# Optimization experiments

Hardware: AMD Instinct MI355X
Metric: run time of the kernel (lower is better)

Reference implementation:

```python
import jax, jax.numpy as jnp
import numpy as np

EPS = 1e-6
H, HKV, D = 32, 8, 64          # heads, kv heads, head_dim
E, TOP_K, FF = 8, 2, 1024      # experts, top-k, expert intermediate
HID = 2048


def rms_norm(x, w):
    xf = x.astype(jnp.float32)
    var = jnp.mean(xf * xf, axis=-1, keepdims=True)
    return (w * (xf * jax.lax.rsqrt(var + EPS)).astype(x.dtype))


def rotate_half(x):
    x1, x2 = jnp.split(x, 2, axis=-1)
    return jnp.concatenate([-x2, x1], axis=-1)


def apply_rope(q, k, cos, sin):
    # cos/sin: [B,S,rd] -> [B,1,S,rd]
    cos = cos[:, None, :, :]
    sin = sin[:, None, :, :]
    rd = cos.shape[-1]
    q_rot, q_pass = q[..., :rd], q[..., rd:]
    k_rot, k_pass = k[..., :rd], k[..., rd:]
    q_emb = q_rot * cos + rotate_half(q_rot) * sin
    k_emb = k_rot * cos + rotate_half(k_rot) * sin
    return (jnp.concatenate([q_emb, q_pass], -1), jnp.concatenate([k_emb, k_pass], -1))


def attention(x, cos, sin, wq, wk, wv, wo):
    B, S, _ = x.shape
    q = (x @ wq).reshape(B, S, H, D).transpose(0, 2, 1, 3)      # [B,H,S,D]
    k = (x @ wk).reshape(B, S, HKV, D).transpose(0, 2, 1, 3)    # [B,Hk,S,D]
    v = (x @ wv).reshape(B, S, HKV, D).transpose(0, 2, 1, 3)
    q, k = apply_rope(q, k, cos, sin)
    rep = H // HKV
    k = jnp.repeat(k, rep, axis=1)
    v = jnp.repeat(v, rep, axis=1)
    scale = D ** -0.5
    scores = jnp.einsum('bhqd,bhkd->bhqk', q, k) * scale
    causal = jnp.triu(jnp.full((S, S), -jnp.inf, dtype=scores.dtype), k=1)
    scores = scores + causal
    probs = jax.nn.softmax(scores.astype(jnp.float32), axis=-1).astype(q.dtype)
    out = jnp.einsum('bhqk,bhkd->bhqd', probs, v)
    out = out.transpose(0, 2, 1, 3).reshape(B, S, H * D)
    return out @ wo


def moe(x, gate_w, corr_bias, w1, w2, w3):
    B, S, Dm = x.shape
    xf = x.reshape(-1, Dm)                                      # [T, Dm]
    T = xf.shape[0]
    logits = xf @ gate_w                                        # [T, E]
    rw = jax.nn.sigmoid(logits.astype(jnp.float32))
    scores = rw + corr_bias
    _, sel = jax.lax.top_k(scores, TOP_K)                       # [T, k]
    tw = jnp.take_along_axis(rw, sel, axis=-1)
    tw = tw / jnp.sum(tw, axis=-1, keepdims=True)
    # dense [T, E] combine weights (zero for unselected experts)
    cw = jnp.zeros((T, E), dtype=xf.dtype).at[jnp.arange(T)[:, None], sel].set(tw.astype(xf.dtype))
    # run every expert densely, combine with sparse weights (same math as gather/scatter loop)
    h = jax.nn.silu(jnp.einsum('td,edf->etf', xf, w1)) * jnp.einsum('td,edf->etf', xf, w3)
    eo = jnp.einsum('etf,efd->etd', h, w2)                      # [E, T, Dm]
    out = jnp.einsum('etd,te->td', eo, cw)
    return out.reshape(B, S, Dm)


def setup_inputs() -> dict:
    key = jax.random.key(0)
    ks = jax.random.split(key, 16)
    s = 0.02
    return {
        'hidden_states': jax.random.normal(ks[0], (2, 1024, HID), jnp.float32),
        'cos': jax.random.uniform(ks[1], (2, 1024, D), jnp.float32),
        'sin': jax.random.uniform(ks[2], (2, 1024, D), jnp.float32),
        'ln1_w': jnp.ones((HID,), jnp.float32),
        'ln2_w': jnp.ones((HID,), jnp.float32),
        'wq': jax.random.normal(ks[3], (HID, H * D), jnp.float32) * s,
        'wk': jax.random.normal(ks[4], (HID, HKV * D), jnp.float32) * s,
        'wv': jax.random.normal(ks[5], (HID, HKV * D), jnp.float32) * s,
        'wo': jax.random.normal(ks[6], (H * D, HID), jnp.float32) * s,
        'gate_w': jax.random.normal(ks[7], (HID, E), jnp.float32) * s,
        'corr_bias': jnp.zeros((E,), jnp.float32),
        'w1': jax.random.normal(ks[8], (E, HID, FF), jnp.float32) * s,
        'w2': jax.random.normal(ks[9], (E, FF, HID), jnp.float32) * s,
        'w3': jax.random.normal(ks[10], (E, HID, FF), jnp.float32) * s,
    }


def reference(hidden_states, cos, sin, ln1_w, ln2_w, wq, wk, wv, wo, gate_w, corr_bias, w1, w2, w3):
    residual = hidden_states
    h = rms_norm(hidden_states, ln1_w)
    h = attention(h, cos, sin, wq, wk, wv, wo)
    h = residual + h
    residual = h
    h = rms_norm(h, ln2_w)
    h = moe(h, gate_w, corr_bias, w1, w2, w3)
    return residual + h
```

## Files before the change

### kernel.cpp

```cpp
#include <hip/hip_runtime.h>
#include <hip/hip_bf16.h>

#define DEV static __device__ __forceinline__

typedef __attribute__((ext_vector_type(8))) short short8;
typedef __attribute__((ext_vector_type(4))) short short4s;
typedef __attribute__((ext_vector_type(8))) __bf16 bf16x8;
typedef __attribute__((ext_vector_type(4))) float floatx4;

DEV short f2bf(float f) {
  unsigned u = __builtin_bit_cast(unsigned, f);
  unsigned r = (u + 0x7fffu + ((u >> 16) & 1u)) >> 16;
  return (short)(unsigned short)r;
}
DEV float bf2f(short s) {
  unsigned u = ((unsigned)(unsigned short)s) << 16;
  return __builtin_bit_cast(float, u);
}
DEV floatx4 mfma16(short8 a, short8 b, floatx4 c) {
  return __builtin_amdgcn_mfma_f32_16x16x32_bf16(
      __builtin_bit_cast(bf16x8, a), __builtin_bit_cast(bf16x8, b), c, 0, 0, 0);
}

#define VMCNT(n) asm volatile("s_waitcnt vmcnt(" #n ")" ::: "memory")
#define SBAR() __builtin_amdgcn_s_barrier()

DEV int sw2(int r) { return (r ^ (r >> 2)) & 3; }

DEV const short* sbase(const short* src, int ld, int row0, int id) {
  int r = id >> 2, cc = id & 3;
  return src + (long)(row0 + r) * ld + ((cc ^ sw2(r)) << 3);
}
DEV void sissue(short* ldsbuf, const short* base, int k0, int tid, int slotbase) {
  int wave = tid >> 6;
  __builtin_amdgcn_global_load_lds(
      (const __attribute__((address_space(1))) void*)(base + k0),
      (__attribute__((address_space(3))) void*)(ldsbuf + (slotbase + wave * 64) * 8),
      16, 0, 0);
}
DEV short8 rdfrag(const short* lds, int row, int l4) {
  return *(const short8*)(lds + row * 32 + ((l4 ^ sw2(row)) << 3));
}

DEV const short* sb64(const short* src, int ld, int row0, int id) {
  int r = id >> 3, c = id & 7;
  return src + (long)(row0 + r) * ld + ((c ^ (r & 7)) << 3);
}
DEV const short* sb64g(const short* src, int ld, const int* rows, int p0, int plim,
                       int id) {
  int r = id >> 3, c = id & 7;
  int pi = p0 + r;
  if (pi > plim) pi = plim;
  return src + (long)rows[pi] * ld + ((c ^ (r & 7)) << 3);
}
DEV short8 rd64(const short* lds, int row, int ch) {
  return *(const short8*)(lds + row * 64 + ((ch ^ (row & 7)) << 3));
}

__global__ __launch_bounds__(256) void k_gemm_qkv(
    const short* Ah, const short* Al, const short* Bh, const short* Bl,
    short* qbh, short* qbl, short* kbh, short* kbl, short* vth, short* vtl,
    const float* cs, const float* sn) {
  const int K = 2048;
  __shared__ __align__(16) short AsH[2][2048], AsL[2][2048], BsH[2][4096], BsL[2][4096];
  int tid = threadIdx.x, lane = tid & 63, wave = tid >> 6;
  int l15 = lane & 15, l4 = lane >> 4;
  int wm = wave >> 1, wn = wave & 1;
  int bid = blockIdx.y * 24 + blockIdx.x;
  int swz = (bid & 7) * 96 + (bid >> 3);
  int bx = swz % 24, by = swz / 24;
  int m0 = by * 64, n0 = bx * 128;

  const short* bA_H = sbase(Ah, K, m0, tid);
  const short* bA_L = sbase(Al, K, m0, tid);
  const short* bBH0 = sbase(Bh, K, n0, tid);
  const short* bBH1 = sbase(Bh, K, n0, tid + 256);
  const short* bBL0 = sbase(Bl, K, n0, tid);
  const short* bBL1 = sbase(Bl, K, n0, tid + 256);

  auto STAGE = [&](int buf, int k0) {
    sissue(AsH[buf], bA_H, k0, tid, 0);
    sissue(AsL[buf], bA_L, k0, tid, 0);
    sissue(BsH[buf], bBH0, k0, tid, 0);
    sissue(BsH[buf], bBH1, k0, tid, 256);
    sissue(BsL[buf], bBL0, k0, tid, 0);
    sissue(BsL[buf], bBL1, k0, tid, 256);
  };

  floatx4 zero4 = {0.f, 0.f, 0.f, 0.f};
  floatx4 acc[2][4];
#pragma unroll
  for (int i = 0; i < 2; ++i)
#pragma unroll
    for (int j = 0; j < 4; ++j) acc[i][j] = zero4;

  STAGE(0, 0);
  STAGE(1, 32);
  int cur = 0;
  for (int k0 = 0; k0 < K; k0 += 32) {
    if (k0 + 64 < K) VMCNT(6); else VMCNT(0);
    SBAR();
    short8 ah[2], al[2], bh2[4], bl2[4];
#pragma unroll
    for (int mi = 0; mi < 2; ++mi) {
      ah[mi] = rdfrag(AsH[cur], wm * 32 + mi * 16 + l15, l4);
      al[mi] = rdfrag(AsL[cur], wm * 32 + mi * 16 + l15, l4);
    }
#pragma unroll
    for (int nt = 0; nt < 4; ++nt) {
      bh2[nt] = rdfrag(BsH[cur], wn * 64 + nt * 16 + l15, l4);
      bl2[nt] = rdfrag(BsL[cur], wn * 64 + nt * 16 + l15, l4);
    }
#pragma unroll
    for (int mi = 0; mi < 2; ++mi)
#pragma unroll
      for (int nt = 0; nt < 4; ++nt) {
        acc[mi][nt] = mfma16(al[mi], bh2[nt], acc[mi][nt]);
        acc[mi][nt] = mfma16(ah[mi], bl2[nt], acc[mi][nt]);
        acc[mi][nt] = mfma16(ah[mi], bh2[nt], acc[mi][nt]);
      }
    SBAR();
    if (k0 + 64 < K) STAGE(cur, k0 + 64);
    cur ^= 1;
  }

  int p = (n0 >> 6) + wn;
  bool isq = p < 32, isk = (!isq) && p < 40;
  if (isq || isk) {
#pragma unroll
    for (int mi = 0; mi < 2; ++mi)
#pragma unroll
      for (int ntp = 0; ntp < 2; ++ntp)
#pragma unroll
        for (int j = 0; j < 4; ++j) {
          int row = m0 + wm * 32 + mi * 16 + l4 * 4 + j;
          int d = ntp * 16 + l15;
          float x0 = acc[mi][ntp][j], x1 = acc[mi][ntp + 2][j];
          float c0 = cs[row * 64 + d], c1 = cs[row * 64 + d + 32];
          float s0 = sn[row * 64 + d], s1 = sn[row * 64 + d + 32];
          float y0 = x0 * c0 - x1 * s0;
          float y1 = x1 * c1 + x0 * s1;
          if (isq) { y0 *= 0.125f; y1 *= 0.125f; }
          acc[mi][ntp][j] = y0;
          acc[mi][ntp + 2][j] = y1;
        }
    short* Ch; short* Cl; int ldc, coff;
    if (isq) { Ch = qbh; Cl = qbl; ldc = 2048; coff = p * 64; }
    else     { Ch = kbh; Cl = kbl; ldc = 512;  coff = (p - 32) * 64; }
#pragma unroll
    for (int mi = 0; mi < 2; ++mi)
#pragma unroll
      for (int nt = 0; nt < 4; ++nt) {
        int row = m0 + wm * 32 + mi * 16 + l4 * 4;
        int col = coff + nt * 16 + l15;
#pragma unroll
        for (int j = 0; j < 4; ++j) {
          float v = acc[mi][nt][j];
          long ix = (long)(row + j) * ldc + col;
          short hi = f2bf(v);
          Ch[ix] = hi;
          Cl[ix] = f2bf(v - bf2f(hi));
        }
      }
  } else {
    int kvh = p - 40;
#pragma unroll
    for (int mi = 0; mi < 2; ++mi)
#pragma unroll
      for (int nt = 0; nt < 4; ++nt) {
        int row0 = m0 + wm * 32 + mi * 16 + l4 * 4;
        int d = nt * 16 + l15;
        int bb = row0 >> 10, tt = row0 & 1023;
        long base = ((long)(bb * 8 + kvh)) * 65536 + (long)d * 1024 + tt;
        short4s hv, lv;
#pragma unroll
        for (int j = 0; j < 4; ++j) {
          float v = acc[mi][nt][j];
          short hi = f2bf(v);
          hv[j] = hi;
          lv[j] = f2bf(v - bf2f(hi));
        }
        *(short4s*)(vth + base) = hv;
        *(short4s*)(vtl + base) = lv;
      }
  }
}

__global__ __launch_bounds__(256) void k_gemm_wo(const short* Ah, const short* Al,
                                                 const short* Bh, const short* Bl,
                                                 const float* resid, float* out) {
  const int K = 2048;
  __shared__ __align__(16) short AsH[2][4096], AsL[2][4096], BsH[2][2048], BsL[2][2048];
  int tid = threadIdx.x, lane = tid & 63, wave = tid >> 6;
  int l15 = lane & 15, l4 = lane >> 4;
  int bid = blockIdx.y * 32 + blockIdx.x;
  int swz = (bid & 7) * 64 + (bid >> 3);
  int bx = swz % 32, by = swz / 32;
  int m0 = by * 128, n0 = bx * 64;

  const short* bAH0 = sbase(Ah, K, m0, tid);
  const short* bAH1 = sbase(Ah, K, m0, tid + 256);
  const short* bAL0 = sbase(Al, K, m0, tid);
  const short* bAL1 = sbase(Al, K, m0, tid + 256);
  const short* bBH0 = sbase(Bh, K, n0, tid);
  const short* bBL0 = sbase(Bl, K, n0, tid);

  auto STAGE = [&](int buf, int k0) {
    sissue(AsH[buf], bAH0, k0, tid, 0);
    sissue(AsH[buf], bAH1, k0, tid, 256);
    sissue(AsL[buf], bAL0, k0, tid, 0);
    sissue(AsL[buf], bAL1, k0, tid, 256);
    sissue(BsH[buf], bBH0, k0, tid, 0);
    sissue(BsL[buf], bBL0, k0, tid, 0);
  };

  floatx4 zero4 = {0.f, 0.f, 0.f, 0.f};
  floatx4 acc[2][4];
#pragma unroll
  for (int i = 0; i < 2; ++i)
#pragma unroll
    for (int j = 0; j < 4; ++j) acc[i][j] = zero4;

  STAGE(0, 0);
  STAGE(1, 32);
  int cur = 0;
  for (int k0 = 0; k0 < K; k0 += 32) {
    if (k0 + 64 < K) VMCNT(6); else VMCNT(0);
    SBAR();
    short8 ah[2], al[2], bh2[4], bl2[4];
#pragma unroll
    for (int mi = 0; mi < 2; ++mi) {
      ah[mi] = rdfrag(AsH[cur], wave * 32 + mi * 16 + l15, l4);
      al[mi] = rdfrag(AsL[cur], wave * 32 + mi * 16 + l15, l4);
    }
#pragma unroll
    for (int nt = 0; nt < 4; ++nt) {
      bh2[nt] = rdfrag(BsH[cur], nt * 16 + l15, l4);
      bl2[nt] = rdfrag(BsL[cur], nt * 16 + l15, l4);
    }
#pragma unroll
    for (int mi = 0; mi < 2; ++mi)
#pragma unroll
      for (int nt = 0; nt < 4; ++nt) {
        acc[mi][nt] = mfma16(al[mi], bh2[nt], acc[mi][nt]);
        acc[mi][nt] = mfma16(ah[mi], bl2[nt], acc[mi][nt]);
        acc[mi][nt] = mfma16(ah[mi], bh2[nt], acc[mi][nt]);
      }
    SBAR();
    if (k0 + 64 < K) STAGE(cur, k0 + 64);
    cur ^= 1;
  }
#pragma unroll
  for (int mi = 0; mi < 2; ++mi)
#pragma unroll
    for (int nt = 0; nt < 4; ++nt) {
      int row = m0 + wave * 32 + mi * 16 + l4 * 4;
      int col = n0 + nt * 16 + l15;
#pragma unroll
      for (int j = 0; j < 4; ++j) {
        long ix = (long)(row + j) * 2048 + col;
        out[ix] = resid[ix] + acc[mi][nt][j];
      }
    }
}

__global__ __launch_bounds__(256) void k_moe_a(const short* X, const short* W1T,
                                               const short* W3T, const int* rows,
                                               const int* cnt, const int* eoff,
                                               short* hh) {
  int e = blockIdx.z;
  int c = cnt[e];
  int mtile = blockIdx.y;
  if (mtile * 128 >= c) return;
  int p0 = eoff[e] + mtile * 128;
  int plim = eoff[e] + c - 1;
  const short* B1 = W1T + (long)e * 1024 * 2048;
  const short* B3 = W3T + (long)e * 1024 * 2048;
  int n0 = blockIdx.x * 64;
  __shared__ __align__(16) short As_[2][8192], B1s[2][4096], B3s[2][4096];
  int tid = threadIdx.x, lane = tid & 63, wave = tid >> 6;
  int l15 = lane & 15, l4 = lane >> 4;
  int wm = wave >> 1, wn = wave & 1;

  const short* bA0 = sb64g(X, 2048, rows, p0, plim, tid);
  const short* bA1 = sb64g(X, 2048, rows, p0, plim, tid + 256);
  const short* bA2 = sb64g(X, 2048, rows, p0, plim, tid + 512);
  const short* bA3 = sb64g(X, 2048, rows, p0, plim, tid + 768);
  const short* bB1_0 = sb64(B1, 2048, n0, tid);
  const short* bB1_1 = sb64(B1, 2048, n0, tid + 256);
  const short* bB3_0 = sb64(B3, 2048, n0, tid);
  const short* bB3_1 = sb64(B3, 2048, n0, tid + 256);

  auto STAGE = [&](int buf, int k0) {
    sissue(As_[buf], bA0, k0, tid, 0);
    sissue(As_[buf], bA1, k0, tid, 256);
    sissue(As_[buf], bA2, k0, tid, 512);
    sissue(As_[buf], bA3, k0, tid, 768);
    sissue(B1s[buf], bB1_0, k0, tid, 0);
    sissue(B1s[buf], bB1_1, k0, tid, 256);
    sissue(B3s[buf], bB3_0, k0, tid, 0);
    sissue(B3s[buf], bB3_1, k0, tid, 256);
  };

  floatx4 zero4 = {0.f, 0.f, 0.f, 0.f};
  floatx4 acc1[4][2], acc3[4][2];
#pragma unroll
  for (int i = 0; i < 4; ++i)
#pragma unroll
    for (int j = 0; j < 2; ++j) { acc1[i][j] = zero4; acc3[i][j] = zero4; }

  STAGE(0, 0);
  STAGE(1, 64);
  int cur = 0;
  for (int k0 = 0; k0 < 2048; k0 += 64) {
    if (k0 + 128 < 2048) VMCNT(8); else VMCNT(0);
    SBAR();
#pragma unroll
    for (int kh = 0; kh < 2; ++kh) {
      int ch = kh * 4 + l4;
      short8 af[4], b1f[2], b3f[2];
#pragma unroll
      for (int mi = 0; mi < 4; ++mi)
        af[mi] = rd64(As_[cur], wm * 64 + mi * 16 + l15, ch);
#pragma unroll
      for (int nt = 0; nt < 2; ++nt) {
        b1f[nt] = rd64(B1s[cur], wn * 32 + nt * 16 + l15, ch);
        b3f[nt] = rd64(B3s[cur], wn * 32 + nt * 16 + l15, ch);
      }
#pragma unroll
      for (int mi = 0; mi < 4; ++mi)
#pragma unroll
        for (int nt = 0; nt < 2; ++nt) {
          acc1[mi][nt] = mfma16(af[mi], b1f[nt], acc1[mi][nt]);
          acc3[mi][nt] = mfma16(af[mi], b3f[nt], acc3[mi][nt]);
        }
    }
    SBAR();
    if (k0 + 128 < 2048) STAGE(cur, k0 + 128);
    cur ^= 1;
  }
#pragma unroll
  for (int mi = 0; mi < 4; ++mi)
#pragma unroll
    for (int nt = 0; nt < 2; ++nt) {
      int col = n0 + wn * 32 + nt * 16 + l15;
#pragma unroll
      for (int j = 0; j < 4; ++j) {
        int rl = wm * 64 + mi * 16 + l4 * 4 + j;
        if (mtile * 128 + rl < c) {
          float v1 = acc1[mi][nt][j], v3 = acc3[mi][nt][j];
          float hg = v1 / (1.f + __expf(-v1));
          hh[(long)(p0 + rl) * 1024 + col] = f2bf(hg * v3);
        }
      }
    }
}

__global__ __launch_bounds__(256) void k_moe_b(const short* hh, const short* W2T,
                                               const int* cnt, const int* eoff,
                                               short* mo) {
  int e = blockIdx.z;
  int c = cnt[e];
  int mtile = blockIdx.y;
  if (mtile * 128 >= c) return;
  int p0 = eoff[e] + mtile * 128;
  const short* B = W2T + (long)e * 2048 * 1024;
  int n0 = blockIdx.x * 128;
  __shared__ __align__(16) short As_[2][8192], Bs_[2][8192];
  int tid = threadIdx.x, lane = tid & 63, wave = tid >> 6;
  int l15 = lane & 15, l4 = lane >> 4;
  int wm = wave >> 1, wn = wave & 1;

  const short* bA0 = sb64(hh, 1024, p0, tid);
  const short* bA1 = sb64(hh, 1024, p0, tid + 256);
  const short* bA2 = sb64(hh, 1024, p0, tid + 512);
  const short* bA3 = sb64(hh, 1024, p0, tid + 768);
  const short* bB0 = sb64(B, 1024, n0, tid);
  const short* bB1 = sb64(B, 1024, n0, tid + 256);
  const short* bB2 = sb64(B, 1024, n0, tid + 512);
  const short* bB3 = sb64(B, 1024, n0, tid + 768);

  auto STAGE = [&](int buf, int k0) {
    sissue(As_[buf], bA0, k0, tid, 0);
    sissue(As_[buf], bA1, k0, tid, 256);
    sissue(As_[buf], bA2, k0, tid, 512);
    sissue(As_[buf], bA3, k0, tid, 768);
    sissue(Bs_[buf], bB0, k0, tid, 0);
    sissue(Bs_[buf], bB1, k0, tid, 256);
    sissue(Bs_[buf], bB2, k0, tid, 512);
    sissue(Bs_[buf], bB3, k0, tid, 768);
  };

  floatx4 zero4 = {0.f, 0.f, 0.f, 0.f};
  floatx4 acc[4][4];
#pragma unroll
  for (int i = 0; i < 4; ++i)
#pragma unroll
    for (int j = 0; j < 4; ++j) acc[i][j] = zero4;

  STAGE(0, 0);
  STAGE(1, 64);
  int cur = 0;
  for (int k0 = 0; k0 < 1024; k0 += 64) {
    if (k0 + 128 < 1024) VMCNT(8); else VMCNT(0);
    SBAR();
#pragma unroll
    for (int kh = 0; kh < 2; ++kh) {
      int ch = kh * 4 + l4;
      short8 af[4], bfv[4];
#pragma unroll
      for (int mi = 0; mi < 4; ++mi)
        af[mi] = rd64(As_[cur], wm * 64 + mi * 16 + l15, ch);
#pragma unroll
      for (int nt = 0; nt < 4; ++nt)
        bfv[nt] = rd64(Bs_[cur], wn * 64 + nt * 16 + l15, ch);
#pragma unroll
      for (int mi = 0; mi < 4; ++mi)
#pragma unroll
        for (int nt = 0; nt < 4; ++nt)
          acc[mi][nt] = mfma16(af[mi], bfv[nt], acc[mi][nt]);
    }
    SBAR();
    if (k0 + 128 < 1024) STAGE(cur, k0 + 128);
    cur ^= 1;
  }
#pragma unroll
  for (int mi = 0; mi < 4; ++mi)
#pragma unroll
    for (int nt = 0; nt < 4; ++nt) {
      int col = n0 + wn * 64 + nt * 16 + l15;
#pragma unroll
      for (int j = 0; j < 4; ++j) {
        int rl = wm * 64 + mi * 16 + l4 * 4 + j;
        if (mtile * 128 + rl < c) mo[(long)(p0 + rl) * 2048 + col] = f2bf(acc[mi][nt][j]);
      }
    }
}

DEV int vsw(int r) { return (r ^ (r >> 3)) & 7; }
DEV short8 avread(const short* buf, int row, int c) {
  return *(const short8*)(buf + row * 64 + (((c ^ vsw(row)) & 7) << 3));
}
DEV int aswz(int r, int c) { return r * 64 + (((c ^ ((r ^ (r >> 3)) & 7)) & 7) << 3); }
DEV void glds(short* ldsslot, const short* src) {
  __builtin_amdgcn_global_load_lds(
      (const __attribute__((address_space(1))) void*)src,
      (__attribute__((address_space(3))) void*)ldsslot, 16, 0, 0);
}

__global__ __launch_bounds__(256) void k_attn3(
    const short* qhp, const short* qlp, const short* khp, const short* klp,
    const short* vth2, const short* vtl2, short* oh, short* ol) {
  int xp = blockIdx.x, bh = blockIdx.y;
  int h = bh & 31, b = bh >> 5, kvh = h >> 2;
  int tid = threadIdx.x, wave = tid >> 6, lane = tid & 63;
  int l15 = lane & 15, l4 = lane >> 4;
  int qtA = 15 - xp, qtB = xp;

  __shared__ __align__(16) short Kh[2][4096], Kl[2][4096], Vh[2][4096], Vl[2][4096];
  __shared__ __align__(16) short Ph[4][1024], Pl[4][1024];

  short8 qh[2][2], ql[2][2];
#pragma unroll
  for (int tt = 0; tt < 2; ++tt) {
    int qrow = (tt ? qtB : qtA) * 64 + wave * 16 + l15;
    long qoff = ((long)(b * 1024 + qrow)) * 2048 + h * 64;
    qh[tt][0] = *(const short8*)(qhp + qoff + l4 * 8);
    qh[tt][1] = *(const short8*)(qhp + qoff + 32 + l4 * 8);
    ql[tt][0] = *(const short8*)(qlp + qoff + l4 * 8);
    ql[tt][1] = *(const short8*)(qlp + qoff + 32 + l4 * 8);
  }

  floatx4 zero4 = {0.f, 0.f, 0.f, 0.f};
  floatx4 acco[2][4];
  float mrun[2][4], lrun[2][4];
#pragma unroll
  for (int tt = 0; tt < 2; ++tt)
#pragma unroll
    for (int j = 0; j < 4; ++j) {
      acco[tt][j] = zero4;
      mrun[tt][j] = -1e30f;
      lrun[tt][j] = 0.f;
    }

  const short* khb = khp + ((long)b * 1024) * 512 + kvh * 64;
  const short* klb = klp + ((long)b * 1024) * 512 + kvh * 64;
  const short* vhb = vth2 + (long)(b * 8 + kvh) * 65536;
  const short* vlb = vtl2 + (long)(b * 8 + kvh) * 65536;

  int r0 = tid >> 3, c0 = tid & 7;
  int r1 = r0 + 32;
  const short* kh0 = khb + (long)r0 * 512 + ((c0 ^ vsw(r0)) << 3);
  const short* kh1 = khb + (long)r1 * 512 + ((c0 ^ vsw(r1)) << 3);
  const short* kl0 = klb + (long)r0 * 512 + ((c0 ^ vsw(r0)) << 3);
  const short* kl1 = klb + (long)r1 * 512 + ((c0 ^ vsw(r1)) << 3);
  const short* vh0 = vhb + (long)r0 * 1024 + ((c0 ^ vsw(r0)) << 3);
  const short* vh1 = vhb + (long)r1 * 1024 + ((c0 ^ vsw(r1)) << 3);
  const short* vl0 = vlb + (long)r0 * 1024 + ((c0 ^ vsw(r0)) << 3);
  const short* vl1 = vlb + (long)r1 * 1024 + ((c0 ^ vsw(r1)) << 3);
  int wslot = wave * 512;

  auto STAGE = [&](int buf, int kt) {
    int ko = kt * 32768;
    int vo = kt * 64;
    glds(&Kh[buf][wslot], kh0 + ko);
    glds(&Kh[buf][2048 + wslot], kh1 + ko);
    glds(&Kl[buf][wslot], kl0 + ko);
    glds(&Kl[buf][2048 + wslot], kl1 + ko);
    glds(&Vh[buf][wslot], vh0 + vo);
    glds(&Vh[buf][2048 + wslot], vh1 + vo);
    glds(&Vl[buf][wslot], vl0 + vo);
    glds(&Vl[buf][2048 + wslot], vl1 + vo);
  };

  STAGE(0, 0);
  int cur = 0;
  for (int kt = 0; kt <= qtA; ++kt) {
    __syncthreads();
    if (kt < qtA) STAGE(cur ^ 1, kt + 1);
#pragma unroll
    for (int tt = 0; tt < 2; ++tt) {
      int qtt = tt ? qtB : qtA;
      if (tt == 1 && kt > qtB) continue;
      floatx4 accs[4] = {zero4, zero4, zero4, zero4};
      __builtin_amdgcn_s_setprio(1);
#pragma unroll
      for (int ks = 0; ks < 2; ++ks) {
        short8 qah = qh[tt][ks];
        short8 qal = ql[tt][ks];
#pragma unroll
        for (int nt = 0; nt < 4; ++nt) {
          int kvr = nt * 16 + l15;
          short8 kfh = avread(Kh[cur], kvr, l4 + 4 * ks);
          short8 kfl = avread(Kl[cur], kvr, l4 + 4 * ks);
          accs[nt] = mfma16(qal, kfh, accs[nt]);
          accs[nt] = mfma16(qah, kfl, accs[nt]);
          accs[nt] = mfma16(qah, kfh, accs[nt]);
        }
      }
      __builtin_amdgcn_s_setprio(0);
      if (kt == qtt) {
#pragma unroll
        for (int nt = 0; nt < 4; ++nt)
#pragma unroll
          for (int j = 0; j < 4; ++j) {
            int kvg = nt * 16 + l15;
            int qg = wave * 16 + l4 * 4 + j;
            if (kvg > qg) accs[nt][j] = -1e30f;
          }
      }
      float pj[4][4];
#pragma unroll
      for (int j = 0; j < 4; ++j) {
        float mx = fmaxf(fmaxf(accs[0][j], accs[1][j]), fmaxf(accs[2][j], accs[3][j]));
        mx = fmaxf(mx, __shfl_xor(mx, 1));
        mx = fmaxf(mx, __shfl_xor(mx, 2));
        mx = fmaxf(mx, __shfl_xor(mx, 4));
        mx = fmaxf(mx, __shfl_xor(mx, 8));
        float mnew = fmaxf(mrun[tt][j], mx);
        float alpha = __expf(mrun[tt][j] - mnew);
        float rs = 0.f;
#pragma unroll
        for (int nt = 0; nt < 4; ++nt) {
          float pv = __expf(accs[nt][j] - mnew);
          pj[nt][j] = pv;
          rs += pv;
        }
        rs += __shfl_xor(rs, 1);
        rs += __shfl_xor(rs, 2);
        rs += __shfl_xor(rs, 4);
        rs += __shfl_xor(rs, 8);
        lrun[tt][j] = lrun[tt][j] * alpha + rs;
        mrun[tt][j] = mnew;
        acco[tt][0][j] *= alpha; acco[tt][1][j] *= alpha;
        acco[tt][2][j] *= alpha; acco[tt][3][j] *= alpha;
      }
      short* P = Ph[wave];
      short* P2 = Pl[wave];
#pragma unroll
      for (int nt = 0; nt < 4; ++nt)
#pragma unroll
        for (int j = 0; j < 4; ++j) {
          int rr = l4 * 4 + j, col = nt * 16 + l15;
          float pv = pj[nt][j];
          short hi = f2bf(pv);
          int ad = aswz(rr, col >> 3) + (col & 7);
          P[ad] = hi;
          P2[ad] = f2bf(pv - bf2f(hi));
        }
      asm volatile("s_waitcnt lgkmcnt(0)" ::: "memory");
      __builtin_amdgcn_sched_barrier(0);
      __builtin_amdgcn_s_setprio(1);
#pragma unroll
      for (int ks = 0; ks < 2; ++ks) {
        short8 pah = *(const short8*)(P + aswz(l15, l4 + 4 * ks));
        short8 pal = *(const short8*)(P2 + aswz(l15, l4 + 4 * ks));
#pragma unroll
        for (int nt = 0; nt < 4; ++nt) {
          int dr = nt * 16 + l15;
          short8 vfh = avread(Vh[cur], dr, l4 + 4 * ks);
          short8 vfl = avread(Vl[cur], dr, l4 + 4 * ks);
          acco[tt][nt] = mfma16(pal, vfh, acco[tt][nt]);
          acco[tt][nt] = mfma16(pah, vfl, acco[tt][nt]);
          acco[tt][nt] = mfma16(pah, vfh, acco[tt][nt]);
        }
      }
      __builtin_amdgcn_s_setprio(0);
    }
    cur ^= 1;
  }
#pragma unroll
  for (int tt = 0; tt < 2; ++tt) {
    int qtt = tt ? qtB : qtA;
#pragma unroll
    for (int j = 0; j < 4; ++j) {
      float invl = 1.f / lrun[tt][j];
      int qg = qtt * 64 + wave * 16 + l4 * 4 + j;
      long ooff = ((long)(b * 1024 + qg)) * 2048 + h * 64;
#pragma unroll
      for (int nt = 0; nt < 4; ++nt) {
        float v = acco[tt][nt][j] * invl;
        short hi = f2bf(v);
        oh[ooff + nt * 16 + l15] = hi;
        ol[ooff + nt * 16 + l15] = f2bf(v - bf2f(hi));
      }
    }
  }
}

DEV void trans_load(const float* src, int N, int n0, int k0, float (*t)[65], int tid) {
  int r = tid >> 2, cq = tid & 3;
  const float* s = src + (long)(k0 + r) * N + n0 + cq * 16;
#pragma unroll
  for (int i = 0; i < 4; ++i) {
    float4 v = *(const float4*)(s + i * 4);
    t[r][cq * 16 + i * 4 + 0] = v.x;
    t[r][cq * 16 + i * 4 + 1] = v.y;
    t[r][cq * 16 + i * 4 + 2] = v.z;
    t[r][cq * 16 + i * 4 + 3] = v.w;
  }
}

DEV void trans_tile1(const float* src, short* dst, int N, int K, int n0, int k0,
                     float (*t)[65]) {
  int tid = threadIdx.x;
  trans_load(src, N, n0, k0, t, tid);
  __syncthreads();
  int n = tid >> 2, kc = tid & 3;
#pragma unroll
  for (int ii = 0; ii < 2; ++ii) {
    short8 o;
#pragma unroll
    for (int j = 0; j < 8; ++j) o[j] = f2bf(t[kc * 16 + ii * 8 + j][n]);
    *(short8*)(dst + (long)(n0 + n) * K + k0 + kc * 16 + ii * 8) = o;
  }
}

DEV void trans_tile2(const float* src, short* dh, short* dl, int N, int K, int n0,
                     int k0, float (*t)[65]) {
  int tid = threadIdx.x;
  trans_load(src, N, n0, k0, t, tid);
  __syncthreads();
  int n = tid >> 2, kc = tid & 3;
#pragma unroll
  for (int ii = 0; ii < 2; ++ii) {
    short8 ohv, olv;
#pragma unroll
    for (int j = 0; j < 8; ++j) {
      float v = t[kc * 16 + ii * 8 + j][n];
      short hi = f2bf(v);
      ohv[j] = hi;
      olv[j] = f2bf(v - bf2f(hi));
    }
    *(short8*)(dh + (long)(n0 + n) * K + k0 + kc * 16 + ii * 8) = ohv;
    *(short8*)(dl + (long)(n0 + n) * K + k0 + kc * 16 + ii * 8) = olv;
  }
}

__global__ __launch_bounds__(256) void k_trans_all(
    const float* wq, const float* wk, const float* wv, const float* wo,
    const float* w1, const float* w3, const float* w2,
    short* qkvTh, short* qkvTl, short* woTh, short* woTl,
    short* w1T, short* w3T, short* w2T,
    const float* x, const float* ln1, short* hbh, short* hbl) {
  __shared__ float t[64][65];
  __shared__ float red[4];
  int bid = blockIdx.x;
  if (bid < 2560) {
    int xx = bid % 80, kt = bid / 80;
    const float* src; short* dh; short* dl; int N, n0;
    if (xx < 32)      { src = wq; dh = qkvTh; dl = qkvTl; N = 2048; n0 = xx * 64; }
    else if (xx < 40) { src = wk; dh = qkvTh + 2048L * 2048; dl = qkvTl + 2048L * 2048;
                        N = 512; n0 = (xx - 32) * 64; }
    else if (xx < 48) { src = wv; dh = qkvTh + 2560L * 2048; dl = qkvTl + 2560L * 2048;
                        N = 512; n0 = (xx - 40) * 64; }
    else              { src = wo; dh = woTh; dl = woTl; N = 2048; n0 = (xx - 48) * 64; }
    trans_tile2(src, dh, dl, N, 2048, n0, kt * 64, t);
  } else if (bid < 10752) {
    int i = bid - 2560;
    int xx = i % 256, kt = i / 256;
    const float* src; short* dst; int n0;
    if (xx < 128) { int e = xx >> 4; src = w1 + (long)e * 2048 * 1024;
                    dst = w1T + (long)e * 1024 * 2048; n0 = (xx & 15) * 64; }
    else          { int x2 = xx - 128, e = x2 >> 4; src = w3 + (long)e * 2048 * 1024;
                    dst = w3T + (long)e * 1024 * 2048; n0 = (x2 & 15) * 64; }
    trans_tile1(src, dst, 1024, 2048, n0, kt * 64, t);
  } else if (bid < 14848) {
    int i = bid - 10752;
    int xx = i % 256, kt = i / 256;
    int e = xx >> 5, ntb = xx & 31;
    trans_tile1(w2 + (long)e * 1024 * 2048, w2T + (long)e * 2048 * 1024,
                2048, 1024, ntb * 64, kt * 64, t);
  } else {
    int row = bid - 14848, tid = threadIdx.x;
    const float* xr = x + (long)row * 2048;
    float4 a = *(const float4*)(xr + tid * 8);
    float4 c = *(const float4*)(xr + tid * 8 + 4);
    float ss = a.x * a.x + a.y * a.y + a.z * a.z + a.w * a.w +
               c.x * c.x + c.y * c.y + c.z * c.z + c.w * c.w;
    ss += __shfl_xor(ss, 1);  ss += __shfl_xor(ss, 2);  ss += __shfl_xor(ss, 4);
    ss += __shfl_xor(ss, 8);  ss += __shfl_xor(ss, 16); ss += __shfl_xor(ss, 32);
    int wave = tid >> 6;
    if ((tid & 63) == 0) red[wave] = ss;
    __syncthreads();
    float tot = red[0] + red[1] + red[2] + red[3];
    float inv = 1.f / sqrtf(tot * (1.f / 2048.f) + 1e-6f);
    float4 w0 = *(const float4*)(ln1 + tid * 8);
    float4 w1v = *(const float4*)(ln1 + tid * 8 + 4);
    float xv[8] = {a.x * w0.x, a.y * w0.y, a.z * w0.z, a.w * w0.w,
                   c.x * w1v.x, c.y * w1v.y, c.z * w1v.z, c.w * w1v.w};
    short8 ohv, olv;
#pragma unroll
    for (int j = 0; j < 8; ++j) {
      float v = xv[j] * inv;
      short hi = f2bf(v);
      ohv[j] = hi;
      olv[j] = f2bf(v - bf2f(hi));
    }
    *(short8*)(hbh + (long)row * 2048 + tid * 8) = ohv;
    *(short8*)(hbl + (long)row * 2048 + tid * 8) = olv;
  }
}

__global__ __launch_bounds__(256) void k_rmsnorm2_gate(const float* x, const float* w,
                                                       const float* gw, const float* cb,
                                                       short* out, int* sel, float* tw,
                                                       int* cnt) {
  int row = blockIdx.x, tid = threadIdx.x;
  const float* xr = x + (long)row * 2048;
  float4 a = *(const float4*)(xr + tid * 8);
  float4 c = *(const float4*)(xr + tid * 8 + 4);
  float ss = a.x * a.x + a.y * a.y + a.z * a.z + a.w * a.w +
             c.x * c.x + c.y * c.y + c.z * c.z + c.w * c.w;
  ss += __shfl_xor(ss, 1);  ss += __shfl_xor(ss, 2);  ss += __shfl_xor(ss, 4);
  ss += __shfl_xor(ss, 8);  ss += __shfl_xor(ss, 16); ss += __shfl_xor(ss, 32);
  __shared__ float red[4];
  int wave = tid >> 6;
  if ((tid & 63) == 0) red[wave] = ss;
  __syncthreads();
  float tot = red[0] + red[1] + red[2] + red[3];
  float inv = 1.f / sqrtf(tot * (1.f / 2048.f) + 1e-6f);
  float4 w0 = *(const float4*)(w + tid * 8);
  float4 w1 = *(const float4*)(w + tid * 8 + 4);
  float xn[8];
  xn[0] = a.x * inv * w0.x; xn[1] = a.y * inv * w0.y; xn[2] = a.z * inv * w0.z;
  xn[3] = a.w * inv * w0.w; xn[4] = c.x * inv * w1.x; xn[5] = c.y * inv * w1.y;
  xn[6] = c.z * inv * w1.z; xn[7] = c.w * inv * w1.w;
  short8 o;
#pragma unroll
  for (int j = 0; j < 8; ++j) o[j] = f2bf(xn[j]);
  *(short8*)(out + (long)row * 2048 + tid * 8) = o;
  float gp[8] = {0.f, 0.f, 0.f, 0.f, 0.f, 0.f, 0.f, 0.f};
#pragma unroll
  for (int j = 0; j < 8; ++j) {
    const float* g = gw + (long)(tid * 8 + j) * 8;
    float4 g0 = *(const float4*)g;
    float4 g1 = *(const float4*)(g + 4);
    gp[0] += xn[j] * g0.x; gp[1] += xn[j] * g0.y; gp[2] += xn[j] * g0.z; gp[3] += xn[j] * g0.w;
    gp[4] += xn[j] * g1.x; gp[5] += xn[j] * g1.y; gp[6] += xn[j] * g1.z; gp[7] += xn[j] * g1.w;
  }
#pragma unroll
  for (int e = 0; e < 8; ++e) {
    gp[e] += __shfl_xor(gp[e], 1);  gp[e] += __shfl_xor(gp[e], 2);
    gp[e] += __shfl_xor(gp[e], 4);  gp[e] += __shfl_xor(gp[e], 8);
    gp[e] += __shfl_xor(gp[e], 16); gp[e] += __shfl_xor(gp[e], 32);
  }
  __shared__ float gred[4][8];
  __shared__ float srw[8], ssc[8];
  if ((tid & 63) == 0) {
#pragma unroll
    for (int e = 0; e < 8; ++e) gred[wave][e] = gp[e];
  }
  __syncthreads();
  if (tid < 8) {
    float lg = gred[0][tid] + gred[1][tid] + gred[2][tid] + gred[3][tid];
    float rw = 1.f / (1.f + expf(-lg));
    srw[tid] = rw;
    ssc[tid] = rw + cb[tid];
  }
  __syncthreads();
  if (tid == 0) {
    int e0 = 0; float b0 = ssc[0];
    for (int e = 1; e < 8; ++e) if (ssc[e] > b0) { b0 = ssc[e]; e0 = e; }
    int e1 = -1; float b1 = -1e30f;
    for (int e = 0; e < 8; ++e) if (e != e0 && ssc[e] > b1) { b1 = ssc[e]; e1 = e; }
    float t0 = srw[e0], t1 = srw[e1], s = t0 + t1;
    sel[row * 2] = e0; sel[row * 2 + 1] = e1;
    tw[row * 2] = t0 / s; tw[row * 2 + 1] = t1 / s;
    atomicAdd(&cnt[e0], 1);
    atomicAdd(&cnt[e1], 1);
  }
}

__global__ __launch_bounds__(256) void k_scan_scatter(const int* cnt, int* eoff,
                                                      int* fill, const int* sel,
                                                      int* rows, int* pos) {
  if (threadIdx.x == 0) {
    int s = 0;
    for (int e = 0; e < 8; ++e) { eoff[e] = s; s += cnt[e]; }
  }
  __syncthreads();
  for (int base = 0; base < 2048; base += 256) {
    int t = base + threadIdx.x;
    for (int k = 0; k < 2; ++k) {
      int e = sel[t * 2 + k];
      int p = eoff[e] + atomicAdd(&fill[e], 1);
      rows[p] = t;
      pos[t * 2 + k] = p;
    }
  }
}

__global__ __launch_bounds__(256) void k_combine(float* out, const short* mo,
                                                 const int* pos, const float* tw) {
  int t = blockIdx.x, tid = threadIdx.x;
  int p0 = pos[t * 2], p1 = pos[t * 2 + 1];
  float w0 = tw[t * 2], w1 = tw[t * 2 + 1];
  float* o = out + (long)t * 2048 + tid * 8;
  short8 m0 = *(const short8*)(mo + (long)p0 * 2048 + tid * 8);
  short8 m1 = *(const short8*)(mo + (long)p1 * 2048 + tid * 8);
  float4 a = *(const float4*)o;
  float4 b = *(const float4*)(o + 4);
  a.x += w0 * bf2f(m0[0]) + w1 * bf2f(m1[0]);
  a.y += w0 * bf2f(m0[1]) + w1 * bf2f(m1[1]);
  a.z += w0 * bf2f(m0[2]) + w1 * bf2f(m1[2]);
  a.w += w0 * bf2f(m0[3]) + w1 * bf2f(m1[3]);
  b.x += w0 * bf2f(m0[4]) + w1 * bf2f(m1[4]);
  b.y += w0 * bf2f(m0[5]) + w1 * bf2f(m1[5]);
  b.z += w0 * bf2f(m0[6]) + w1 * bf2f(m1[6]);
  b.w += w0 * bf2f(m0[7]) + w1 * bf2f(m1[7]);
  *(float4*)o = a;
  *(float4*)(o + 4) = b;
}

extern "C" void kernel_launch(void* const* d_in, const int* in_sizes, int n_in,
                              void* d_out, int out_size, void* d_ws, size_t ws_size,
                              hipStream_t stream) {
  const float* x    = (const float*)d_in[0];
  const float* cosb = (const float*)d_in[1];
  const float* sinb = (const float*)d_in[2];
  const float* ln1  = (const float*)d_in[3];
  const float* ln2  = (const float*)d_in[4];
  const float* wq   = (const float*)d_in[5];
  const float* wk   = (const float*)d_in[6];
  const float* wv   = (const float*)d_in[7];
  const float* wo   = (const float*)d_in[8];
  const float* gw   = (const float*)d_in[9];
  const float* cb   = (const float*)d_in[10];
  const float* w1   = (const float*)d_in[11];
  const float* w2   = (const float*)d_in[12];
  const float* w3   = (const float*)d_in[13];
  float* out = (float*)d_out;

  char* p = (char*)d_ws;
  auto take = [&](size_t n) { char* r = p; p += (n + 255) & ~(size_t)255; return r; };
  short* qkvTh = (short*)take(3072L * 2048 * 2);
  short* qkvTl = (short*)take(3072L * 2048 * 2);
  short* woTh  = (short*)take(2048L * 2048 * 2);
  short* woTl  = (short*)take(2048L * 2048 * 2);
  short* w1T   = (short*)take(8L * 1024 * 2048 * 2);
  short* w3T   = (short*)take(8L * 1024 * 2048 * 2);
  short* w2T   = (short*)take(8L * 2048 * 1024 * 2);
  short* hbh   = (short*)take(2048L * 2048 * 2);
  short* hbl   = (short*)take(2048L * 2048 * 2);
  short* qbh   = (short*)take(2048L * 2048 * 2);
  short* qbl   = (short*)take(2048L * 2048 * 2);
  short* kbh   = (short*)take(2048L * 512 * 2);
  short* kbl   = (short*)take(2048L * 512 * 2);
  short* vth   = (short*)take(16L * 64 * 1024 * 2);
  short* vtl   = (short*)take(16L * 64 * 1024 * 2);
  short* aoh   = (short*)take(2048L * 2048 * 2);
  short* aol   = (short*)take(2048L * 2048 * 2);
  short* h2b   = (short*)take(2048L * 2048 * 2);
  short* hhb   = (short*)take(4224L * 1024 * 2);
  short* mob   = (short*)take(4352L * 2048 * 2);
  int* rti     = (int*)take(64 * sizeof(int));
  int* cnt = rti; int* fill = rti + 8; int* eoff = rti + 16;
  int* sel     = (int*)take(2048L * 2 * 4);
  float* twb   = (float*)take(2048L * 2 * 4);
  int* rowsp   = (int*)take(4352L * 4);
  int* posb    = (int*)take(2048L * 2 * 4);
  (void)ws_size; (void)in_sizes; (void)n_in; (void)out_size;

  dim3 B256(256);
  k_trans_all<<<dim3(16896), B256, 0, stream>>>(wq, wk, wv, wo, w1, w3, w2,
                                                qkvTh, qkvTl, woTh, woTl,
                                                w1T, w3T, w2T, x, ln1, hbh, hbl);
  hipMemsetAsync(rti, 0, 64, stream);

  k_gemm_qkv<<<dim3(24, 32), B256, 0, stream>>>(hbh, hbl, qkvTh, qkvTl, qbh, qbl,
                                                kbh, kbl, vth, vtl, cosb, sinb);
  k_attn3<<<dim3(8, 64), B256, 0, stream>>>(qbh, qbl, kbh, kbl, vth, vtl, aoh, aol);
  k_gemm_wo<<<dim3(32, 16), B256, 0, stream>>>(aoh, aol, woTh, woTl, x, out);

  k_rmsnorm2_gate<<<dim3(2048), B256, 0, stream>>>(out, ln2, gw, cb, h2b, sel, twb, cnt);
  k_scan_scatter<<<dim3(1), B256, 0, stream>>>(cnt, eoff, fill, sel, rowsp, posb);
  k_moe_a<<<dim3(16, 16, 8), B256, 0, stream>>>(h2b, w1T, w3T, rowsp, cnt, eoff, hhb);
  k_moe_b<<<dim3(16, 16, 8), B256, 0, stream>>>(hhb, w2T, cnt, eoff, mob);
  k_combine<<<dim3(2048), B256, 0, stream>>>(out, mob, posb, twb);
}
```

Before: 544.6 us.

## Overlap weight transposes with QKV GEMM and attention via block interleaving

Splits the monolithic weight-transpose kernel so that only the QKV weights and the first RMSNorm run up front. The Wo transpose is folded into the QKV GEMM launch (4 of every 7 blocks) and the MoE expert transposes into the attention launch (24 of every 25 blocks). This is meant to fill idle CUs during the compute-bound GEMM and attention phases with memory-bound transpose work, hiding its cost. In exchange, LDS is a fixed-size shared char buffer sized for the largest role, which may lower occupancy for the transpose blocks. The compute blocks also now compete for bandwidth with the transposes.

```diff
diff --git a/kernel.cpp b/kernel.cpp
--- a/kernel.cpp
+++ b/kernel.cpp
@@ -57,17 +57,127 @@
   return *(const short8*)(lds + row * 64 + ((ch ^ (row & 7)) << 3));
 }
 
-__global__ __launch_bounds__(256) void k_gemm_qkv(
+DEV void trans_load(const float* src, int N, int n0, int k0, float (*t)[65], int tid) {
+  int r = tid >> 2, cq = tid & 3;
+  const float* s = src + (long)(k0 + r) * N + n0 + cq * 16;
+#pragma unroll
+  for (int i = 0; i < 4; ++i) {
+    float4 v = *(const float4*)(s + i * 4);
+    t[r][cq * 16 + i * 4 + 0] = v.x;
+    t[r][cq * 16 + i * 4 + 1] = v.y;
+    t[r][cq * 16 + i * 4 + 2] = v.z;
+    t[r][cq * 16 + i * 4 + 3] = v.w;
+  }
+}
+
+DEV void trans_tile1(const float* src, short* dst, int N, int K, int n0, int k0,
+                     float (*t)[65]) {
+  int tid = threadIdx.x;
+  trans_load(src, N, n0, k0, t, tid);
+  __syncthreads();
+  int n = tid >> 2, kc = tid & 3;
+#pragma unroll
+  for (int ii = 0; ii < 2; ++ii) {
+    short8 o;
+#pragma unroll
+    for (int j = 0; j < 8; ++j) o[j] = f2bf(t[kc * 16 + ii * 8 + j][n]);
+    *(short8*)(dst + (long)(n0 + n) * K + k0 + kc * 16 + ii * 8) = o;
+  }
+}
+
+DEV void trans_tile2(const float* src, short* dh, short* dl, int N, int K, int n0,
+                     int k0, float (*t)[65]) {
+  int tid = threadIdx.x;
+  trans_load(src, N, n0, k0, t, tid);
+  __syncthreads();
+  int n = tid >> 2, kc = tid & 3;
+#pragma unroll
+  for (int ii = 0; ii < 2; ++ii) {
+    short8 ohv, olv;
+#pragma unroll
+    for (int j = 0; j < 8; ++j) {
+      float v = t[kc * 16 + ii * 8 + j][n];
+      short hi = f2bf(v);
+      ohv[j] = hi;
+      olv[j] = f2bf(v - bf2f(hi));
+    }
+    *(short8*)(dh + (long)(n0 + n) * K + k0 + kc * 16 + ii * 8) = ohv;
+    *(short8*)(dl + (long)(n0 + n) * K + k0 + kc * 16 + ii * 8) = olv;
+  }
+}
+
+__global__ __launch_bounds__(256) void k_trans_pre(
+    const float* wq, const float* wk, const float* wv,
+    short* qkvTh, short* qkvTl,
+    const float* x, const float* ln1, short* hbh, short* hbl) {
+  __shared__ float t[64][65];
+  __shared__ float red[4];
+  int bid = blockIdx.x;
+  if (bid < 1536) {
+    int xx = bid % 48, kt = bid / 48;
+    const float* src; short* dh; short* dl; int N, n0;
+    if (xx < 32)      { src = wq; dh = qkvTh; dl = qkvTl; N = 2048; n0 = xx * 64; }
+    else if (xx < 40) { src = wk; dh = qkvTh + 2048L * 2048; dl = qkvTl + 2048L * 2048;
+                        N = 512; n0 = (xx - 32) * 64; }
+    else              { src = wv; dh = qkvTh + 2560L * 2048; dl = qkvTl + 2560L * 2048;
+                        N = 512; n0 = (xx - 40) * 64; }
+    trans_tile2(src, dh, dl, N, 2048, n0, kt * 64, t);
+  } else {
+    int row = bid - 1536, tid = threadIdx.x;
+    const float* xr = x + (long)row * 2048;
+    float4 a = *(const float4*)(xr + tid * 8);
+    float4 c = *(const float4*)(xr + tid * 8 + 4);
+    float ss = a.x * a.x + a.y * a.y + a.z * a.z + a.w * a.w +
+               c.x * c.x + c.y * c.y + c.z * c.z + c.w * c.w;
+    ss += __shfl_xor(ss, 1);  ss += __shfl_xor(ss, 2);  ss += __shfl_xor(ss, 4);
+    ss += __shfl_xor(ss, 8);  ss += __shfl_xor(ss, 16); ss += __shfl_xor(ss, 32);
+    int wave = tid >> 6;
+    if ((tid & 63) == 0) red[wave] = ss;
+    __syncthreads();
+    float tot = red[0] + red[1] + red[2] + red[3];
+    float inv = 1.f / sqrtf(tot * (1.f / 2048.f) + 1e-6f);
+    float4 w0 = *(const float4*)(ln1 + tid * 8);
+    float4 w1v = *(const float4*)(ln1 + tid * 8 + 4);
+    float xv[8] = {a.x * w0.x, a.y * w0.y, a.z * w0.z, a.w * w0.w,
+                   c.x * w1v.x, c.y * w1v.y, c.z * w1v.z, c.w * w1v.w};
+    short8 ohv, olv;
+#pragma unroll
+    for (int j = 0; j < 8; ++j) {
+      float v = xv[j] * inv;
+      short hi = f2bf(v);
+      ohv[j] = hi;
+      olv[j] = f2bf(v - bf2f(hi));
+    }
+    *(short8*)(hbh + (long)row * 2048 + tid * 8) = ohv;
+    *(short8*)(hbl + (long)row * 2048 + tid * 8) = olv;
+  }
+}
+
+__global__ __launch_bounds__(256) void k_qkv_plus(
     const short* Ah, const short* Al, const short* Bh, const short* Bl,
     short* qbh, short* qbl, short* kbh, short* kbl, short* vth, short* vtl,
-    const float* cs, const float* sn) {
+    const float* cs, const float* sn,
+    const float* wo, short* woTh, short* woTl) {
+  __shared__ __align__(16) char smem[49152];
+  int gbid = blockIdx.x;
+  int grp = gbid / 7, rem = gbid % 7;
+  if (rem >= 3) {
+    float (*t)[65] = (float(*)[65])smem;
+    int wi = grp * 4 + (rem - 3);
+    int xx = wi % 32, kt = wi / 32;
+    trans_tile2(wo, woTh, woTl, 2048, 2048, xx * 64, kt * 64, t);
+    return;
+  }
+  int qi = grp * 3 + rem;
   const int K = 2048;
-  __shared__ __align__(16) short AsH[2][2048], AsL[2][2048], BsH[2][4096], BsL[2][4096];
+  short* AsH = (short*)smem;
+  short* AsL = AsH + 4096;
+  short* BsH = AsL + 4096;
+  short* BsL = BsH + 8192;
   int tid = threadIdx.x, lane = tid & 63, wave = tid >> 6;
   int l15 = lane & 15, l4 = lane >> 4;
   int wm = wave >> 1, wn = wave & 1;
-  int bid = blockIdx.y * 24 + blockIdx.x;
-  int swz = (bid & 7) * 96 + (bid >> 3);
+  int swz = (qi & 7) * 96 + (qi >> 3);
   int bx = swz % 24, by = swz / 24;
   int m0 = by * 64, n0 = bx * 128;
 
@@ -79,12 +189,12 @@
   const short* bBL1 = sbase(Bl, K, n0, tid + 256);
 
   auto STAGE = [&](int buf, int k0) {
-    sissue(AsH[buf], bA_H, k0, tid, 0);
-    sissue(AsL[buf], bA_L, k0, tid, 0);
-    sissue(BsH[buf], bBH0, k0, tid, 0);
-    sissue(BsH[buf], bBH1, k0, tid, 256);
-    sissue(BsL[buf], bBL0, k0, tid, 0);
-    sissue(BsL[buf], bBL1, k0, tid, 256);
+    sissue(AsH + buf * 2048, bA_H, k0, tid, 0);
+    sissue(AsL + buf * 2048, bA_L, k0, tid, 0);
+    sissue(BsH + buf * 4096, bBH0, k0, tid, 0);
+    sissue(BsH + buf * 4096, bBH1, k0, tid, 256);
+    sissue(BsL + buf * 4096, bBL0, k0, tid, 0);
+    sissue(BsL + buf * 4096, bBL1, k0, tid, 256);
   };
 
   floatx4 zero4 = {0.f, 0.f, 0.f, 0.f};
@@ -103,13 +213,13 @@
     short8 ah[2], al[2], bh2[4], bl2[4];
 #pragma unroll
     for (int mi = 0; mi < 2; ++mi) {
-      ah[mi] = rdfrag(AsH[cur], wm * 32 + mi * 16 + l15, l4);
-      al[mi] = rdfrag(AsL[cur], wm * 32 + mi * 16 + l15, l4);
+      ah[mi] = rdfrag(AsH + cur * 2048, wm * 32 + mi * 16 + l15, l4);
+      al[mi] = rdfrag(AsL + cur * 2048, wm * 32 + mi * 16 + l15, l4);
     }
 #pragma unroll
     for (int nt = 0; nt < 4; ++nt) {
-      bh2[nt] = rdfrag(BsH[cur], wn * 64 + nt * 16 + l15, l4);
-      bl2[nt] = rdfrag(BsL[cur], wn * 64 + nt * 16 + l15, l4);
+      bh2[nt] = rdfrag(BsH + cur * 4096, wn * 64 + nt * 16 + l15, l4);
+      bl2[nt] = rdfrag(BsL + cur * 4096, wn * 64 + nt * 16 + l15, l4);
     }
 #pragma unroll
     for (int mi = 0; mi < 2; ++mi)
@@ -448,17 +558,47 @@
       (__attribute__((address_space(3))) void*)ldsslot, 16, 0, 0);
 }
 
-__global__ __launch_bounds__(256) void k_attn3(
+__global__ __launch_bounds__(256) void k_attn_plus(
     const short* qhp, const short* qlp, const short* khp, const short* klp,
-    const short* vth2, const short* vtl2, short* oh, short* ol) {
-  int xp = blockIdx.x, bh = blockIdx.y;
+    const short* vth2, const short* vtl2, short* oh, short* ol,
+    const float* w1, const float* w3, const float* w2,
+    short* w1T, short* w3T, short* w2T) {
+  __shared__ __align__(16) char smem[81920];
+  int gbid = blockIdx.x;
+  int grp = gbid / 25, rem = gbid % 25;
+  if (rem != 0) {
+    float (*t)[65] = (float(*)[65])smem;
+    int ti = grp * 24 + (rem - 1);
+    if (ti < 8192) {
+      int xx = ti % 256, kt = ti / 256;
+      const float* src; short* dst; int n0;
+      if (xx < 128) { int e = xx >> 4; src = w1 + (long)e * 2048 * 1024;
+                      dst = w1T + (long)e * 1024 * 2048; n0 = (xx & 15) * 64; }
+      else          { int x2 = xx - 128, e = x2 >> 4; src = w3 + (long)e * 2048 * 1024;
+                      dst = w3T + (long)e * 1024 * 2048; n0 = (x2 & 15) * 64; }
+      trans_tile1(src, dst, 1024, 2048, n0, kt * 64, t);
+    } else {
+      int i = ti - 8192;
+      int xx = i % 256, kt = i / 256;
+      int e = xx >> 5, ntb = xx & 31;
+      trans_tile1(w2 + (long)e * 1024 * 2048, w2T + (long)e * 2048 * 1024,
+                  2048, 1024, ntb * 64, kt * 64, t);
+    }
+    return;
+  }
+  int ai = grp;
+  int xp = ai % 8, bh = ai / 8;
   int h = bh & 31, b = bh >> 5, kvh = h >> 2;
   int tid = threadIdx.x, wave = tid >> 6, lane = tid & 63;
   int l15 = lane & 15, l4 = lane >> 4;
   int qtA = 15 - xp, qtB = xp;
 
-  __shared__ __align__(16) short Kh[2][4096], Kl[2][4096], Vh[2][4096], Vl[2][4096];
-  __shared__ __align__(16) short Ph[4][1024], Pl[4][1024];
+  short* Kh = (short*)smem;
+  short* Kl = Kh + 8192;
+  short* Vh = Kl + 8192;
+  short* Vl = Vh + 8192;
+  short* Ph = Vl + 8192;
+  short* Pl = Ph + 4096;
 
   short8 qh[2][2], ql[2][2];
 #pragma unroll
@@ -503,14 +643,14 @@
   auto STAGE = [&](int buf, int kt) {
     int ko = kt * 32768;
     int vo = kt * 64;
-    glds(&Kh[buf][wslot], kh0 + ko);
-    glds(&Kh[buf][2048 + wslot], kh1 + ko);
-    glds(&Kl[buf][wslot], kl0 + ko);
-    glds(&Kl[buf][2048 + wslot], kl1 + ko);
-    glds(&Vh[buf][wslot], vh0 + vo);
-    glds(&Vh[buf][2048 + wslot], vh1 + vo);
-    glds(&Vl[buf][wslot], vl0 + vo);
-    glds(&Vl[buf][2048 + wslot], vl1 + vo);
+    glds(Kh + buf * 4096 + wslot, kh0 + ko);
+    glds(Kh + buf * 4096 + 2048 + wslot, kh1 + ko);
+    glds(Kl + buf * 4096 + wslot, kl0 + ko);
+    glds(Kl + buf * 4096 + 2048 + wslot, kl1 + ko);
+    glds(Vh + buf * 4096 + wslot, vh0 + vo);
+    glds(Vh + buf * 4096 + 2048 + wslot, vh1 + vo);
+    glds(Vl + buf * 4096 + wslot, vl0 + vo);
+    glds(Vl + buf * 4096 + 2048 + wslot, vl1 + vo);
   };
 
   STAGE(0, 0);
@@ -531,8 +671,8 @@
 #pragma unroll
         for (int nt = 0; nt < 4; ++nt) {
           int kvr = nt * 16 + l15;
-          short8 kfh = avread(Kh[cur], kvr, l4 + 4 * ks);
-          short8 kfl = avread(Kl[cur], kvr, l4 + 4 * ks);
+          short8 kfh = avread(Kh + cur * 4096, kvr, l4 + 4 * ks);
+          short8 kfl = avread(Kl + cur * 4096, kvr, l4 + 4 * ks);
           accs[nt] = mfma16(qal, kfh, accs[nt]);
           accs[nt] = mfma16(qah, kfl, accs[nt]);
           accs[nt] = mfma16(qah, kfh, accs[nt]);
@@ -575,8 +715,8 @@
         acco[tt][0][j] *= alpha; acco[tt][1][j] *= alpha;
         acco[tt][2][j] *= alpha; acco[tt][3][j] *= alpha;
       }
-      short* P = Ph[wave];
-      short* P2 = Pl[wave];
+      short* P = Ph + wave * 1024;
+      short* P2 = Pl + wave * 1024;
 #pragma unroll
       for (int nt = 0; nt < 4; ++nt)
 #pragma unroll
@@ -598,8 +738,8 @@
 #pragma unroll
         for (int nt = 0; nt < 4; ++nt) {
           int dr = nt * 16 + l15;
-          short8 vfh = avread(Vh[cur], dr, l4 + 4 * ks);
-          short8 vfl = avread(Vl[cur], dr, l4 + 4 * ks);
+          short8 vfh = avread(Vh + cur * 4096, dr, l4 + 4 * ks);
+          short8 vfl = avread(Vl + cur * 4096, dr, l4 + 4 * ks);
           acco[tt][nt] = mfma16(pal, vfh, acco[tt][nt]);
           acco[tt][nt] = mfma16(pah, vfl, acco[tt][nt]);
           acco[tt][nt] = mfma16(pah, vfh, acco[tt][nt]);
@@ -625,120 +765,6 @@
         ol[ooff + nt * 16 + l15] = f2bf(v - bf2f(hi));
       }
     }
-  }
-}
-
-DEV void trans_load(const float* src, int N, int n0, int k0, float (*t)[65], int tid) {
-  int r = tid >> 2, cq = tid & 3;
-  const float* s = src + (long)(k0 + r) * N + n0 + cq * 16;
-#pragma unroll
-  for (int i = 0; i < 4; ++i) {
-    float4 v = *(const float4*)(s + i * 4);
-    t[r][cq * 16 + i * 4 + 0] = v.x;
-    t[r][cq * 16 + i * 4 + 1] = v.y;
-    t[r][cq * 16 + i * 4 + 2] = v.z;
-    t[r][cq * 16 + i * 4 + 3] = v.w;
-  }
-}
-
-DEV void trans_tile1(const float* src, short* dst, int N, int K, int n0, int k0,
-                     float (*t)[65]) {
-  int tid = threadIdx.x;
-  trans_load(src, N, n0, k0, t, tid);
-  __syncthreads();
-  int n = tid >> 2, kc = tid & 3;
-#pragma unroll
-  for (int ii = 0; ii < 2; ++ii) {
-    short8 o;
-#pragma unroll
-    for (int j = 0; j < 8; ++j) o[j] = f2bf(t[kc * 16 + ii * 8 + j][n]);
-    *(short8*)(dst + (long)(n0 + n) * K + k0 + kc * 16 + ii * 8) = o;
-  }
-}
-
-DEV void trans_tile2(const float* src, short* dh, short* dl, int N, int K, int n0,
-                     int k0, float (*t)[65]) {
-  int tid = threadIdx.x;
-  trans_load(src, N, n0, k0, t, tid);
-  __syncthreads();
-  int n = tid >> 2, kc = tid & 3;
-#pragma unroll
-  for (int ii = 0; ii < 2; ++ii) {
-    short8 ohv, olv;
-#pragma unroll
-    for (int j = 0; j < 8; ++j) {
-      float v = t[kc * 16 + ii * 8 + j][n];
-      short hi = f2bf(v);
-      ohv[j] = hi;
-      olv[j] = f2bf(v - bf2f(hi));
-    }
-    *(short8*)(dh + (long)(n0 + n) * K + k0 + kc * 16 + ii * 8) = ohv;
-    *(short8*)(dl + (long)(n0 + n) * K + k0 + kc * 16 + ii * 8) = olv;
-  }
-}
-
-__global__ __launch_bounds__(256) void k_trans_all(
-    const float* wq, const float* wk, const float* wv, const float* wo,
-    const float* w1, const float* w3, const float* w2,
-    short* qkvTh, short* qkvTl, short* woTh, short* woTl,
-    short* w1T, short* w3T, short* w2T,
-    const float* x, const float* ln1, short* hbh, short* hbl) {
-  __shared__ float t[64][65];
-  __shared__ float red[4];
-  int bid = blockIdx.x;
-  if (bid < 2560) {
-    int xx = bid % 80, kt = bid / 80;
-    const float* src; short* dh; short* dl; int N, n0;
-    if (xx < 32)      { src = wq; dh = qkvTh; dl = qkvTl; N = 2048; n0 = xx * 64; }
-    else if (xx < 40) { src = wk; dh = qkvTh + 2048L * 2048; dl = qkvTl + 2048L * 2048;
-                        N = 512; n0 = (xx - 32) * 64; }
-    else if (xx < 48) { src = wv; dh = qkvTh + 2560L * 2048; dl = qkvTl + 2560L * 2048;
-                        N = 512; n0 = (xx - 40) * 64; }
-    else              { src = wo; dh = woTh; dl = woTl; N = 2048; n0 = (xx - 48) * 64; }
-    trans_tile2(src, dh, dl, N, 2048, n0, kt * 64, t);
-  } else if (bid < 10752) {
-    int i = bid - 2560;
-    int xx = i % 256, kt = i / 256;
-    const float* src; short* dst; int n0;
-    if (xx < 128) { int e = xx >> 4; src = w1 + (long)e * 2048 * 1024;
-                    dst = w1T + (long)e * 1024 * 2048; n0 = (xx & 15) * 64; }
-    else          { int x2 = xx - 128, e = x2 >> 4; src = w3 + (long)e * 2048 * 1024;
-                    dst = w3T + (long)e * 1024 * 2048; n0 = (x2 & 15) * 64; }
-    trans_tile1(src, dst, 1024, 2048, n0, kt * 64, t);
-  } else if (bid < 14848) {
-    int i = bid - 10752;
-    int xx = i % 256, kt = i / 256;
-    int e = xx >> 5, ntb = xx & 31;
-    trans_tile1(w2 + (long)e * 1024 * 2048, w2T + (long)e * 2048 * 1024,
-                2048, 1024, ntb * 64, kt * 64, t);
-  } else {
-    int row = bid - 14848, tid = threadIdx.x;
-    const float* xr = x + (long)row * 2048;
-    float4 a = *(const float4*)(xr + tid * 8);
-    float4 c = *(const float4*)(xr + tid * 8 + 4);
-    float ss = a.x * a.x + a.y * a.y + a.z * a.z + a.w * a.w +
-               c.x * c.x + c.y * c.y + c.z * c.z + c.w * c.w;
-    ss += __shfl_xor(ss, 1);  ss += __shfl_xor(ss, 2);  ss += __shfl_xor(ss, 4);
-    ss += __shfl_xor(ss, 8);  ss += __shfl_xor(ss, 16); ss += __shfl_xor(ss, 32);
-    int wave = tid >> 6;
-    if ((tid & 63) == 0) red[wave] = ss;
-    __syncthreads();
-    float tot = red[0] + red[1] + red[2] + red[3];
-    float inv = 1.f / sqrtf(tot * (1.f / 2048.f) + 1e-6f);
-    float4 w0 = *(const float4*)(ln1 + tid * 8);
-    float4 w1v = *(const float4*)(ln1 + tid * 8 + 4);
-    float xv[8] = {a.x * w0.x, a.y * w0.y, a.z * w0.z, a.w * w0.w,
-                   c.x * w1v.x, c.y * w1v.y, c.z * w1v.z, c.w * w1v.w};
-    short8 ohv, olv;
-#pragma unroll
-    for (int j = 0; j < 8; ++j) {
-      float v = xv[j] * inv;
-      short hi = f2bf(v);
-      ohv[j] = hi;
-      olv[j] = f2bf(v - bf2f(hi));
-    }
-    *(short8*)(hbh + (long)row * 2048 + tid * 8) = ohv;
-    *(short8*)(hbl + (long)row * 2048 + tid * 8) = olv;
   }
 }
 
@@ -903,14 +929,15 @@
   (void)ws_size; (void)in_sizes; (void)n_in; (void)out_size;
 
   dim3 B256(256);
-  k_trans_all<<<dim3(16896), B256, 0, stream>>>(wq, wk, wv, wo, w1, w3, w2,
-                                                qkvTh, qkvTl, woTh, woTl,
-                                                w1T, w3T, w2T, x, ln1, hbh, hbl);
+  k_trans_pre<<<dim3(3584), B256, 0, stream>>>(wq, wk, wv, qkvTh, qkvTl,
+                                               x, ln1, hbh, hbl);
   hipMemsetAsync(rti, 0, 64, stream);
 
-  k_gemm_qkv<<<dim3(24, 32), B256, 0, stream>>>(hbh, hbl, qkvTh, qkvTl, qbh, qbl,
-                                                kbh, kbl, vth, vtl, cosb, sinb);
-  k_attn3<<<dim3(8, 64), B256, 0, stream>>>(qbh, qbl, kbh, kbl, vth, vtl, aoh, aol);
+  k_qkv_plus<<<dim3(1792), B256, 0, stream>>>(hbh, hbl, qkvTh, qkvTl, qbh, qbl,
+                                              kbh, kbl, vth, vtl, cosb, sinb,
+                                              wo, woTh, woTl);
+  k_attn_plus<<<dim3(12800), B256, 0, stream>>>(qbh, qbl, kbh, kbl, vth, vtl,
+                                                aoh, aol, w1, w3, w2, w1T, w3T, w2T);
   k_gemm_wo<<<dim3(32, 16), B256, 0, stream>>>(aoh, aol, woTh, woTl, x, out);
 
   k_rmsnorm2_gate<<<dim3(2048), B256, 0, stream>>>(out, ln2, gw, cb, h2b, sel, twb, cnt);
```

After: 614.9 us. 1.13x slower.
